# Kernel optimization log

Hardware: AMD Instinct MI355X
Metric: run time of the kernel (lower is better)

The kernel has to match this reference:

```python
import jax, jax.numpy as jnp
import numpy as np
from functools import partial

TAU = 2.0
EPS = 1e-5

@jax.custom_vjp
def spike(x):
    # Heaviside spike (x >= 0 -> 1). Surrogate sigmoid grad (alpha=4), matching spikingjelly default.
    return (x >= 0).astype(x.dtype)

def _spike_fwd(x):
    return (x >= 0).astype(x.dtype), x

def _spike_bwd(x, g):
    s = jax.nn.sigmoid(4.0 * x)
    return (4.0 * s * (1.0 - s) * g,)

spike.defvjp(_spike_fwd, _spike_bwd)

def lif(x, v_threshold=1.0):
    # Multi-step LIF over leading time axis. v_reset=0, hard reset, detach_reset.
    def step(v, xt):
        v = v + (xt - v) / TAU
        s = spike(v - v_threshold)
        v = v * (1.0 - jax.lax.stop_gradient(s))  # detached hard reset
        return v, s
    _, s = jax.lax.scan(step, jnp.zeros_like(x[0]), x)
    return s

def bn(x, gamma, beta):
    # BatchNorm1d in training mode over (T*B, C, N): stats over axes (T,B,N) per channel.
    m = x.mean(axis=(0, 1, 3), keepdims=True)
    v = x.var(axis=(0, 1, 3), keepdims=True)
    return (x - m) * jax.lax.rsqrt(v + EPS) * gamma[None, None, :, None] + beta[None, None, :, None]

def conv1x1(x, w, b=None):
    # 1x1 conv1d == channel-mixing GEMM. x: [T,B,C,N], w: [O,C]
    y = jnp.einsum('oc,tbcn->tbon', w, x)
    if b is not None:
        y = y + b[None, None, :, None]
    return y

def setup_inputs() -> dict:
    key = jax.random.key(0)
    ks = jax.random.split(key, 16)
    T, B, C, H, W = 4, 16, 512, 16, 16
    sc = 1.0 / np.sqrt(C)
    inp = {
        'x': jax.random.normal(ks[0], (T, B, C, H, W), dtype=jnp.float32),
        'q_w': jax.random.normal(ks[1], (C, C), dtype=jnp.float32) * sc,
        'q_gamma': jnp.ones((C,), jnp.float32), 'q_beta': jnp.zeros((C,), jnp.float32),
        'k_w': jax.random.normal(ks[2], (C, C), dtype=jnp.float32) * sc,
        'k_gamma': jnp.ones((C,), jnp.float32), 'k_beta': jnp.zeros((C,), jnp.float32),
        'v_w': jax.random.normal(ks[3], (C, C), dtype=jnp.float32) * sc,
        'v_gamma': jnp.ones((C,), jnp.float32), 'v_beta': jnp.zeros((C,), jnp.float32),
        'proj_w': jax.random.normal(ks[4], (C, C), dtype=jnp.float32) * sc,
        'proj_b': jnp.zeros((C,), jnp.float32),
        'proj_gamma': jnp.ones((C,), jnp.float32), 'proj_beta': jnp.zeros((C,), jnp.float32),
    }
    return inp

def reference(x, q_w, q_gamma, q_beta, k_w, k_gamma, k_beta, v_w, v_gamma, v_beta,
              proj_w, proj_b, proj_gamma, proj_beta):
    num_heads = 8
    scale = 0.125
    T, B, C, H, W = x.shape
    N = H * W
    d = C // num_heads
    xf = x.reshape(T, B, C, N)

    def branch(w, gamma, beta):
        s = lif(bn(conv1x1(xf, w), gamma, beta))          # [T,B,C,N] spikes
        # -> [T,B,heads,N,d]
        return s.transpose(0, 1, 3, 2).reshape(T, B, N, num_heads, d).transpose(0, 1, 3, 2, 4)

    q = branch(q_w, q_gamma, q_beta)
    k = branch(k_w, k_gamma, k_beta)
    v = branch(v_w, v_gamma, v_beta)

    kv = jnp.einsum('tbhnd,tbhne->tbhde', k, v)           # [T,B,h,d,d]
    attn = jnp.einsum('tbhnd,tbhde->tbhne', q, kv) * scale  # [T,B,h,N,d]
    attn = attn.transpose(0, 1, 2, 4, 3).reshape(T, B, C, N)
    attn = lif(attn, v_threshold=0.5)

    out = bn(conv1x1(attn, proj_w, proj_b), proj_gamma, proj_beta)
    out = lif(out.reshape(T, B, C, H, W))
    return out
```

## Files before the change

kernel.cpp:

```cpp
#include <hip/hip_runtime.h>
#include <hip/hip_bf16.h>
#include <stdint.h>

#define BCN  (16*512*256)
#define CN   (512*256)
#define NG   64
#define CAP  65536

typedef __attribute__((ext_vector_type(8))) short bf16x8;
typedef __attribute__((ext_vector_type(4))) float f32x4;
typedef __attribute__((ext_vector_type(4))) int   int4v;
typedef unsigned char u8;

__device__ inline ushort f2bf(float x){ union{ __hip_bfloat16 b; ushort u; } z; z.b = __float2bfloat16(x); return z.u; }
__device__ inline float  bf2f(ushort u){ union{ uint i; float f; } z; z.i = (uint)u<<16; return z.f; }

__device__ inline double blk_reduce(double v, double* sh){
  int tid = threadIdx.x; sh[tid] = v; __syncthreads();
  for (int off=128; off>0; off>>=1){ if (tid<off) sh[tid]+=sh[tid+off]; __syncthreads(); }
  double r = sh[0]; __syncthreads(); return r;
}

__global__ __launch_bounds__(256) void guard_fill(float* out, int n){
  int i = blockIdx.x*256+threadIdx.x; if (i<n) out[i] = -1.0f;
}

__global__ __launch_bounds__(256) void w_split(const float* __restrict__ W,
                                               ushort* __restrict__ Whi, ushort* __restrict__ Wlo){
  int i = blockIdx.x*256+threadIdx.x; if (i >= 512*512) return;
  float x = W[i]; ushort h = f2bf(x);
  Whi[i] = h; Wlo[i] = f2bf(x - bf2f(h));
}

__global__ __launch_bounds__(256) void wnorm_k(const float* __restrict__ W, double* __restrict__ wn){
  __shared__ double sh[256];
  int o = blockIdx.x;
  double s = 0.0;
  for (int c = threadIdx.x; c < 512; c += 256){ double w = (double)W[o*512+c]; s += w*w; }
  double t = blk_reduce(s, sh);
  if (threadIdx.x==0) wn[o] = sqrt(t);
}

__global__ __launch_bounds__(256) void xtrans32(const float* __restrict__ X, float* __restrict__ XT){
  __shared__ float lds[64][65];
  const int g = blockIdx.z, c0 = blockIdx.y<<6, n0 = blockIdx.x<<6;
  const int t = threadIdx.x, r = t>>2, q = t&3;
  #pragma unroll
  for (int u4=0; u4<4; ++u4){
    f32x4 v = *(const f32x4*)&X[((size_t)g*512 + c0 + r)*256 + n0 + q*16 + u4*4];
    lds[r][q*16+u4*4+0]=v.x; lds[r][q*16+u4*4+1]=v.y; lds[r][q*16+u4*4+2]=v.z; lds[r][q*16+u4*4+3]=v.w;
  }
  __syncthreads();
  #pragma unroll
  for (int u4=0; u4<4; ++u4){
    f32x4 o;
    o.x = lds[q*16+u4*4+0][r]; o.y = lds[q*16+u4*4+1][r];
    o.z = lds[q*16+u4*4+2][r]; o.w = lds[q*16+u4*4+3][r];
    *(f32x4*)&XT[((size_t)g*256 + n0 + r)*512 + c0 + q*16 + u4*4] = o;
  }
}

__global__ __launch_bounds__(256) void u8_trans(const u8* __restrict__ S, u8* __restrict__ ST){
  __shared__ u8 lds[64][65];
  const int g = blockIdx.z, c0 = blockIdx.y<<6, n0 = blockIdx.x<<6;
  const int t = threadIdx.x, r = t>>2, q = t&3;
  int4v v = *(const int4v*)&S[((size_t)g*512 + c0 + r)*256 + n0 + q*16];
  const u8* pb = (const u8*)&v;
  #pragma unroll
  for (int u=0; u<16; ++u) lds[r][q*16+u] = pb[u];
  __syncthreads();
  u8 ob[16];
  #pragma unroll
  for (int u=0; u<16; ++u) ob[u] = lds[q*16+u][r];
  *(int4v*)&ST[((size_t)g*256 + n0 + r)*512 + c0 + q*16] = *(int4v*)ob;
}

template<typename T>
__global__ __launch_bounds__(256) void colsum_k(const T* __restrict__ X, double* __restrict__ cs){
  __shared__ double sh[256];
  const int c = blockIdx.x;
  double s = 0.0;
  for (int g=0; g<NG; ++g) s += (double)X[((size_t)g*512+c)*256 + threadIdx.x];
  double t = blk_reduce(s, sh);
  if (threadIdx.x==0) cs[c] = t;
}

template<typename T>
__global__ __launch_bounds__(256) void norm_k2(const T* __restrict__ X, double* __restrict__ nrm){
  __shared__ double sh[4][64];
  const int g = blockIdx.x>>2, nq = blockIdx.x&3;
  const int nl = threadIdx.x&63, cg = threadIdx.x>>6;
  const int n = nq*64 + nl;
  double s = 0.0;
  #pragma unroll 4
  for (int c=cg; c<512; c+=4){
    double v = (double)X[((size_t)g*512+c)*256 + n]; s += v*v;
  }
  sh[cg][nl] = s; __syncthreads();
  if (cg==0) nrm[g*256+n] = sqrt(sh[0][nl]+sh[1][nl]+sh[2][nl]+sh[3][nl]);
}

__global__ __launch_bounds__(256, 4) void gramx2t(const float* __restrict__ X, double* __restrict__ Gpart){
  const int ti_tab[36] = {0,1,1,2,2,2,3,3,3,3,4,4,4,4,4,5,5,5,5,5,5,6,6,6,6,6,6,6,7,7,7,7,7,7,7,7};
  const int tj_tab[36] = {0,0,1,0,1,2,0,1,2,3,0,1,2,3,4,0,1,2,3,4,5,0,1,2,3,4,5,6,0,1,2,3,4,5,6,7};
  const int p = blockIdx.x, z = blockIdx.y;
  const int ci0 = ti_tab[p]<<6, cj0 = tj_tab[p]<<6;
  const bool offd = (ci0 != cj0);
  const int tid = threadIdx.x, tx = tid&15, ty = tid>>4;
  __shared__ float A[64][68];
  __shared__ float B[64][68];
  double acc[4][4] = {};

  for (int gg=0; gg<4; ++gg){
    const int g = z*4+gg;
    for (int nc=0; nc<4; ++nc){
      const int n0 = nc<<6;
      __syncthreads();
      { const int r = tid>>2, q = tid&3;
        #pragma unroll
        for (int u=0; u<4; ++u){
          f32x4 va = *(const f32x4*)&X[((size_t)g*512 + ci0 + r)*256 + n0 + q*16 + u*4];
          A[q*16+u*4+0][r]=va.x; A[q*16+u*4+1][r]=va.y; A[q*16+u*4+2][r]=va.z; A[q*16+u*4+3][r]=va.w;
          f32x4 vb = *(const f32x4*)&X[((size_t)g*512 + cj0 + r)*256 + n0 + q*16 + u*4];
          B[q*16+u*4+0][r]=vb.x; B[q*16+u*4+1][r]=vb.y; B[q*16+u*4+2][r]=vb.z; B[q*16+u*4+3][r]=vb.w;
        }
      }
      __syncthreads();
      #pragma unroll 8
      for (int n=0; n<64; ++n){
        const f32x4 af = *(const f32x4*)&A[n][ty*4];
        const f32x4 bf = *(const f32x4*)&B[n][tx*4];
        double a[4] = {(double)af.x,(double)af.y,(double)af.z,(double)af.w};
        double b[4] = {(double)bf.x,(double)bf.y,(double)bf.z,(double)bf.w};
        #pragma unroll
        for (int i=0;i<4;++i)
          #pragma unroll
          for (int j=0;j<4;++j) acc[i][j] = fma(a[i], b[j], acc[i][j]);
      }
    }
  }
  double* Gp = Gpart + (size_t)z*262144;
  #pragma unroll
  for (int i=0;i<4;++i)
    #pragma unroll
    for (int j=0;j<4;++j){
      Gp[(size_t)(ci0+ty*4+i)*512 + cj0+tx*4+j] = acc[i][j];
      if (offd) Gp[(size_t)(cj0+tx*4+j)*512 + ci0+ty*4+i] = acc[i][j];
    }
}

__global__ __launch_bounds__(256) void greduce64(const double* __restrict__ Gpart, double* __restrict__ G){
  const int i = blockIdx.x*256 + threadIdx.x;
  double s = 0.0;
  #pragma unroll
  for (int z=0; z<16; ++z) s += Gpart[(size_t)z*262144 + i];
  G[i] = s;
}

__global__ __launch_bounds__(256) void greduceS(const float* __restrict__ Gspart, float* __restrict__ Gs){
  const int i = blockIdx.x*256 + threadIdx.x;
  float s = 0.0f;
  #pragma unroll
  for (int z=0; z<16; ++z) s += Gspart[(size_t)z*262144 + i];
  Gs[i] = s;
}

template<typename GT>
__global__ __launch_bounds__(256) void mgemm(const float* __restrict__ W, const GT* __restrict__ G,
                                             double* __restrict__ M){
  const int o0 = blockIdx.y<<6, c0 = blockIdx.x<<6;
  const int k0base = blockIdx.z*128;
  __shared__ float  wT[32][68];
  __shared__ double gS[32][66];
  double acc[4][4];
  #pragma unroll
  for (int i=0;i<4;++i)
    #pragma unroll
    for (int j=0;j<4;++j) acc[i][j]=0.0;
  const int tid = threadIdx.x, tx = tid&15, ty = tid>>4;

  for (int kc=0; kc<4; ++kc){
    const int k0 = k0base + kc*32;
    __syncthreads();
    { int r = tid>>2, q = tid&3;
      f32x4 w0 = *(const f32x4*)&W[(size_t)(o0+r)*512 + k0 + q*8];
      f32x4 w1 = *(const f32x4*)&W[(size_t)(o0+r)*512 + k0 + q*8 + 4];
      wT[q*8+0][r]=w0.x; wT[q*8+1][r]=w0.y; wT[q*8+2][r]=w0.z; wT[q*8+3][r]=w0.w;
      wT[q*8+4][r]=w1.x; wT[q*8+5][r]=w1.y; wT[q*8+6][r]=w1.z; wT[q*8+7][r]=w1.w;
      int k = tid>>3, h = tid&7;
      #pragma unroll
      for (int u=0;u<8;++u) gS[k][h*8+u] = (double)G[(size_t)(k0+k)*512 + c0 + h*8 + u];
    }
    __syncthreads();
    #pragma unroll
    for (int k=0;k<32;++k){
      f32x4 aw = *(const f32x4*)&wT[k][ty*4];
      double a[4] = {(double)aw.x,(double)aw.y,(double)aw.z,(double)aw.w};
      double b[4];
      #pragma unroll
      for (int j=0;j<4;++j) b[j] = gS[k][tx*4+j];
      #pragma unroll
      for (int i=0;i<4;++i)
        #pragma unroll
        for (int j=0;j<4;++j) acc[i][j] = fma(a[i], b[j], acc[i][j]);
    }
  }
  #pragma unroll
  for (int i=0;i<4;++i)
    #pragma unroll
    for (int j=0;j<4;++j)
      atomicAdd(&M[(size_t)(o0+ty*4+i)*512 + c0+tx*4+j], acc[i][j]);
}

__global__ __launch_bounds__(256) void finalize_stats(const float* __restrict__ W, const double* __restrict__ M,
                                                      const double* __restrict__ cs,
                                                      const float* __restrict__ gamma, const float* __restrict__ beta,
                                                      double* __restrict__ stats){
  __shared__ double sh[256];
  const int o = blockIdx.x;
  double s1=0.0, s2=0.0;
  for (int c = threadIdx.x; c < 512; c += 256){
    double w = (double)W[(size_t)o*512+c];
    s1 += w*cs[c]; s2 += w*M[(size_t)o*512+c];
  }
  double t1 = blk_reduce(s1, sh);
  double t2 = blk_reduce(s2, sh);
  if (threadIdx.x==0){
    double mean = t1*(1.0/16384.0);
    double var  = t2*(1.0/16384.0) - mean*mean;
    double sc = (double)gamma[o] / sqrt(var + 1e-5);
    stats[o] = sc; stats[512+o] = (double)beta[o] - mean*sc;
  }
}

template<int MODE>
__global__ __launch_bounds__(256) void fgemm(const ushort* __restrict__ Ahi, const ushort* __restrict__ Alo,
                                             const void* __restrict__ Bsrc, float* __restrict__ Y){
  const int g = blockIdx.z, o0 = blockIdx.y<<7, n0 = blockIdx.x<<7;
  const int tid = threadIdx.x, lane = tid&63, wv = tid>>6;
  const int wo = (wv>>1)<<6, wn2 = (wv&1)<<6;
  const int l15 = lane&15, l4 = lane>>4, ss = l4 ^ (lane&3);
  __shared__ __align__(16) ushort L[4][128][32];
  f32x4 acc[4][4];
  #pragma unroll
  for (int i=0;i<4;++i)
    #pragma unroll
    for (int j=0;j<4;++j) acc[i][j] = f32x4{0.f,0.f,0.f,0.f};

  for (int c0=0; c0<512; c0+=32){
    __syncthreads();
    #pragma unroll
    for (int s2=0; s2<2; ++s2){
      int S = tid*2+s2, r = S>>2, q = S&3, qq = q ^ (r&3);
      *(int4v*)&L[0][r][qq*8] = *(const int4v*)&Ahi[(size_t)(o0+r)*512 + c0 + q*8];
      *(int4v*)&L[1][r][qq*8] = *(const int4v*)&Alo[(size_t)(o0+r)*512 + c0 + q*8];
      if (MODE==0){
        const float* B = (const float*)Bsrc;
        f32x4 x0 = *(const f32x4*)&B[((size_t)g*256 + n0 + r)*512 + c0 + q*8];
        f32x4 x1 = *(const f32x4*)&B[((size_t)g*256 + n0 + r)*512 + c0 + q*8 + 4];
        union { ushort us[8]; int4v v; } hiU, loU;
        float xv[8] = {x0.x,x0.y,x0.z,x0.w,x1.x,x1.y,x1.z,x1.w};
        #pragma unroll
        for (int u=0;u<8;++u){ ushort h = f2bf(xv[u]); hiU.us[u]=h; loU.us[u]=f2bf(xv[u]-bf2f(h)); }
        *(int4v*)&L[2][r][qq*8] = hiU.v;
        *(int4v*)&L[3][r][qq*8] = loU.v;
      } else {
        const u8* B = (const u8*)Bsrc;
        uint2 raw = *(const uint2*)&B[((size_t)g*256 + n0 + r)*512 + c0 + q*8];
        union { ushort us[8]; int4v v; } hiU;
        #pragma unroll
        for (int u=0;u<4;++u) hiU.us[u]   = ((raw.x>>(8*u))&255u) ? 0x3F80 : 0;
        #pragma unroll
        for (int u=0;u<4;++u) hiU.us[4+u] = ((raw.y>>(8*u))&255u) ? 0x3F80 : 0;
        *(int4v*)&L[2][r][qq*8] = hiU.v;
      }
    }
    __syncthreads();
    bf16x8 ah[4], al[4], bh[4], bl[4];
    #pragma unroll
    for (int f=0; f<4; ++f){
      int ra = wo + f*16 + l15;
      ah[f] = *(const bf16x8*)&L[0][ra][ss*8];
      al[f] = *(const bf16x8*)&L[1][ra][ss*8];
      int rb = wn2 + f*16 + l15;
      bh[f] = *(const bf16x8*)&L[2][rb][ss*8];
      if (MODE==0) bl[f] = *(const bf16x8*)&L[3][rb][ss*8];
    }
    #pragma unroll
    for (int of=0; of<4; ++of)
      #pragma unroll
      for (int nf=0; nf<4; ++nf){
        acc[of][nf] = __builtin_amdgcn_mfma_f32_16x16x32_bf16(ah[of], bh[nf], acc[of][nf], 0,0,0);
        acc[of][nf] = __builtin_amdgcn_mfma_f32_16x16x32_bf16(al[of], bh[nf], acc[of][nf], 0,0,0);
        if (MODE==0)
          acc[of][nf] = __builtin_amdgcn_mfma_f32_16x16x32_bf16(ah[of], bl[nf], acc[of][nf], 0,0,0);
      }
  }
  #pragma unroll
  for (int of=0; of<4; ++of)
    #pragma unroll
    for (int nf=0; nf<4; ++nf){
      #pragma unroll
      for (int r=0;r<4;++r){
        int o = o0 + wo + of*16 + l4*4 + r;
        int n = n0 + wn2 + nf*16 + l15;
        Y[((size_t)g*512 + o)*256 + n] = acc[of][nf][r];
      }
    }
}

__global__ __launch_bounds__(256) void sgram(const u8* __restrict__ S, float* __restrict__ Gspart){
  const int ci0 = blockIdx.x<<7, cj0 = blockIdx.y<<7, slice = blockIdx.z;
  const int tid = threadIdx.x, lane = tid&63, wv = tid>>6;
  const int wo = (wv>>1)<<6, wn2 = (wv&1)<<6;
  const int l15 = lane&15, l4 = lane>>4, ss = l4 ^ (lane&3);
  __shared__ __align__(16) ushort L[2][128][32];
  f32x4 acc[4][4];
  #pragma unroll
  for (int i=0;i<4;++i)
    #pragma unroll
    for (int j=0;j<4;++j) acc[i][j] = f32x4{0.f,0.f,0.f,0.f};

  for (int gg=0; gg<4; ++gg){
    const int g = slice*4+gg;
    for (int nc=0; nc<8; ++nc){
      const int n0 = nc*32;
      __syncthreads();
      #pragma unroll
      for (int s2=0; s2<2; ++s2){
        int Sl = tid*2+s2, r = Sl>>2, q = Sl&3, qq = q ^ (r&3);
        uint2 ra = *(const uint2*)&S[((size_t)g*512 + ci0 + r)*256 + n0 + q*8];
        uint2 rb = *(const uint2*)&S[((size_t)g*512 + cj0 + r)*256 + n0 + q*8];
        union { ushort us[8]; int4v v; } A, Bv;
        #pragma unroll
        for (int u=0;u<4;++u){ A.us[u]   = ((ra.x>>(8*u))&255u)?0x3F80:0; Bv.us[u]   = ((rb.x>>(8*u))&255u)?0x3F80:0; }
        #pragma unroll
        for (int u=0;u<4;++u){ A.us[4+u] = ((ra.y>>(8*u))&255u)?0x3F80:0; Bv.us[4+u] = ((rb.y>>(8*u))&255u)?0x3F80:0; }
        *(int4v*)&L[0][r][qq*8] = A.v;
        *(int4v*)&L[1][r][qq*8] = Bv.v;
      }
      __syncthreads();
      bf16x8 af[4], bfv[4];
      #pragma unroll
      for (int f=0; f<4; ++f){
        int ra = wo + f*16 + l15;  af[f]  = *(const bf16x8*)&L[0][ra][ss*8];
        int rb = wn2 + f*16 + l15; bfv[f] = *(const bf16x8*)&L[1][rb][ss*8];
      }
      #pragma unroll
      for (int of=0; of<4; ++of)
        #pragma unroll
        for (int nf=0; nf<4; ++nf)
          acc[of][nf] = __builtin_amdgcn_mfma_f32_16x16x32_bf16(af[of], bfv[nf], acc[of][nf], 0,0,0);
    }
  }
  float* Gp = Gspart + (size_t)slice*262144;
  #pragma unroll
  for (int of=0; of<4; ++of)
    #pragma unroll
    for (int nf=0; nf<4; ++nf)
      #pragma unroll
      for (int r=0;r<4;++r){
        int ci = ci0 + wo + of*16 + l4*4 + r;
        int cj = cj0 + wn2 + nf*16 + l15;
        Gp[(size_t)ci*512 + cj] = acc[of][nf][r];
      }
}

template<int OUTF>
__global__ __launch_bounds__(256) void bn_lif_flag(const float* __restrict__ Y, const double* __restrict__ stats,
                                                   const double* __restrict__ wn, const double* __restrict__ xn,
                                                   double K, void* __restrict__ sout,
                                                   uint* __restrict__ list, int* __restrict__ cnt){
  const int idx = blockIdx.x*256 + threadIdx.x;
  const int n = idx & 255, o = (idx>>8) & 511, b = idx>>17;
  const double scale = stats[o], shift = stats[512+o];
  const double kw = K * fabs(scale) * wn[o];
  double v = 0.0, minm = 1e300, bmax = 0.0;
  #pragma unroll
  for (int t=0;t<4;++t){
    const int g = t*16+b;
    const size_t ii = ((size_t)g*512+o)*256 + n;
    double y = (double)Y[ii];
    double Bnd = kw * xn[g*256+n]; bmax = fmax(bmax, Bnd);
    double z = y*scale + shift;
    v = v + (z - v)*0.5;
    double m = fabs(v - 1.0) - 2.0*bmax;
    minm = fmin(minm, m);
    bool sp = (v - 1.0) >= 0.0;
    if (OUTF) ((float*)sout)[ii] = sp ? 1.0f : 0.0f;
    else      ((u8*)sout)[ii]    = sp ? 1 : 0;
    if (sp) v = 0.0;
  }
  if (minm < 0.0){
    int pos = atomicAdd(cnt, 1);
    if (pos < CAP) list[pos] = ((uint)b<<17)|((uint)o<<8)|(uint)n;
  }
}

template<int OUTF>
__global__ __launch_bounds__(256) void recompute(const uint* __restrict__ list, const int* __restrict__ cnt,
                                                 const float* __restrict__ W, const void* __restrict__ Xn,
                                                 const double* __restrict__ stats, void* __restrict__ out){
  const int lane = threadIdx.x & 63;
  const int wv = blockIdx.x*4 + (threadIdx.x>>6);
  int ne = *cnt; if (ne > CAP) ne = CAP;
  for (int e = wv; e < ne; e += gridDim.x*4){
    const uint code = list[e];
    const int b = code>>17, o = (code>>8)&511, n = code&255;
    if (b > 15) continue;
    const double scale = stats[o], shift = stats[512+o];
    double v = 0.0;
    for (int t=0;t<4;++t){
      const int g = t*16+b;
      double y = 0.0;
      #pragma unroll
      for (int i=0;i<8;++i){
        int c = lane + 64*i;
        double w = (double)W[(size_t)o*512 + c];
        double xv;
        if (OUTF) xv = (double)((const u8*)Xn)[((size_t)g*256+n)*512 + c];
        else      xv = (double)((const float*)Xn)[((size_t)g*256+n)*512 + c];
        y = fma(w, xv, y);
      }
      #pragma unroll
      for (int off=32; off>0; off>>=1) y += __shfl_xor(y, off);
      double z = y*scale + shift;
      v = v + (z - v)*0.5;
      bool sp = (v - 1.0) >= 0.0;
      if (lane==0){
        const size_t ii = ((size_t)g*512+o)*256 + n;
        if (OUTF) ((float*)out)[ii] = sp ? 1.0f : 0.0f;
        else      ((u8*)out)[ii]    = sp ? 1 : 0;
      }
      if (sp) v = 0.0;
    }
  }
}

__global__ __launch_bounds__(256) void lif_kernel(const float* __restrict__ Y, double thresh,
                                                  u8* __restrict__ s_u8){
  const size_t idx = (size_t)blockIdx.x * 256 + threadIdx.x;
  double v = 0.0;
  #pragma unroll
  for (int t = 0; t < 4; ++t){
    double z = (double)Y[(size_t)t * BCN + idx];
    v = v + (z - v) * 0.5;
    bool sp = (v - thresh) >= 0.0;
    s_u8[(size_t)t * BCN + idx] = sp ? 1 : 0;
    if (sp) v = 0.0;
  }
}

__global__ __launch_bounds__(256) void attn_kv(const u8* __restrict__ sk, const u8* __restrict__ sv,
                                               float* __restrict__ kv){
  const int blk = blockIdx.x;
  const int tid = threadIdx.x;
  const size_t base = ((size_t)(blk >> 3) * 512 + (size_t)(blk & 7) * 64) * 256;
  __shared__ u8 kS[64][256];
  __shared__ u8 vS[64][256];
  const uint32_t* K32 = (const uint32_t*)(sk + base);
  const uint32_t* V32 = (const uint32_t*)(sv + base);
  uint32_t* kS32 = (uint32_t*)&kS[0][0];
  uint32_t* vS32 = (uint32_t*)&vS[0][0];
  #pragma unroll
  for (int i = 0; i < 16; ++i){ kS32[i*256+tid] = K32[i*256+tid]; vS32[i*256+tid] = V32[i*256+tid]; }
  __syncthreads();
  const int d0 = (tid >> 4) << 2, e0 = (tid & 15) << 2;
  int acc[4][4] = {};
  for (int n = 0; n < 256; ++n){
    int k_[4], v_[4];
    #pragma unroll
    for (int i = 0; i < 4; ++i) k_[i] = kS[d0+i][n];
    #pragma unroll
    for (int j = 0; j < 4; ++j) v_[j] = vS[e0+j][n];
    #pragma unroll
    for (int i = 0; i < 4; ++i)
      #pragma unroll
      for (int j = 0; j < 4; ++j) acc[i][j] += k_[i]*v_[j];
  }
  float* KV = kv + (size_t)blk * 4096;
  #pragma unroll
  for (int i = 0; i < 4; ++i)
    #pragma unroll
    for (int j = 0; j < 4; ++j) KV[(d0+i)*64 + e0+j] = (float)acc[i][j];
}

__global__ __launch_bounds__(256) void attn_qkv(const u8* __restrict__ sq, const float* __restrict__ kv,
                                                float* __restrict__ attn){
  const int blk = blockIdx.x;
  const int tid = threadIdx.x;
  const size_t base = ((size_t)(blk >> 3) * 512 + (size_t)(blk & 7) * 64) * 256;
  __shared__ u8 qS[64][256];
  __shared__ float kvS[64][64];
  const uint32_t* Q32 = (const uint32_t*)(sq + base);
  uint32_t* qS32 = (uint32_t*)&qS[0][0];
  const float* KV = kv + (size_t)blk * 4096;
  #pragma unroll
  for (int i = 0; i < 16; ++i){
    qS32[i*256+tid] = Q32[i*256+tid];
    (&kvS[0][0])[i*256+tid] = KV[i*256+tid];
  }
  __syncthreads();
  const int n = tid;
  float acc[64];
  #pragma unroll
  for (int e = 0; e < 64; ++e) acc[e] = 0.0f;
  for (int d = 0; d < 64; ++d){
    float qf = (float)qS[d][n];
    #pragma unroll
    for (int e = 0; e < 64; ++e) acc[e] = fmaf(qf, kvS[d][e], acc[e]);
  }
  float* A = attn + base;
  #pragma unroll
  for (int e = 0; e < 64; ++e) A[(size_t)e*256 + n] = acc[e]*0.125f;
}

extern "C" void kernel_launch(void* const* d_in, const int* in_sizes, int n_in,
                              void* d_out, int out_size, void* d_ws, size_t ws_size,
                              hipStream_t stream){
  const float* x       = (const float*)d_in[0];
  const float* Wb[4]   = {(const float*)d_in[1], (const float*)d_in[4], (const float*)d_in[7], (const float*)d_in[10]};
  const float* Gm[4]   = {(const float*)d_in[2], (const float*)d_in[5], (const float*)d_in[8], (const float*)d_in[12]};
  const float* Bt[4]   = {(const float*)d_in[3], (const float*)d_in[6], (const float*)d_in[9], (const float*)d_in[13]};

  char* p = (char*)d_ws;
  float* yA   = (float*)p;            p += 33554432;
  u8* s_q     = (u8*)p;               p += 8388608;
  u8* s_k     = (u8*)p;               p += 8388608;
  u8* s_v     = (u8*)p;               p += 8388608;
  u8* s_at    = (u8*)p;               p += 8388608;
  float* XT32 = (float*)p;
  u8* sT      = (u8*)p;               p += 33554432;
  ushort* Whl = (ushort*)p;           p += 4194304;
  float* kvb  = (float*)p;            p += 8388608;
  double* G   = (double*)p;           p += 2097152;
  float* Gs   = (float*)p;            p += 1048576;
  double* M   = (double*)p;           p += 2097152;
  double* colsumX = (double*)p;       p += 4096;
  double* colsumS = (double*)p;       p += 4096;
  double* xnorm   = (double*)p;       p += 131072;
  double* snorm   = (double*)p;       p += 131072;
  double* wn      = (double*)p;       p += 16384;
  double* stats   = (double*)p;       p += 32768;
  int*    cnt     = (int*)p;          p += 256;
  uint*   lists   = (uint*)p;         p += 4*CAP*4;
  const size_t NEED = (size_t)(p - (char*)d_ws);

  double* Gpart  = (double*)yA;
  float*  Gspart = (float*)yA;

  if (ws_size < NEED){
    guard_fill<<<(out_size+255)/256, 256, 0, stream>>>((float*)d_out, out_size);
    return;
  }

  const double K0 = 4.0e-5;
  const double K1 = 4.0e-5;

  hipMemsetAsync(cnt, 0, 256, stream);

  for (int i=0;i<4;++i){
    w_split<<<1024, 256, 0, stream>>>(Wb[i], Whl + (size_t)i*524288, Whl + (size_t)i*524288 + 262144);
    wnorm_k<<<512, 256, 0, stream>>>(Wb[i], wn + i*512);
  }
  xtrans32<<<dim3(4,8,64), 256, 0, stream>>>(x, XT32);
  colsum_k<float><<<512, 256, 0, stream>>>(x, colsumX);
  norm_k2<float><<<256, 256, 0, stream>>>(x, xnorm);
  gramx2t<<<dim3(36,16), 256, 0, stream>>>(x, Gpart);
  greduce64<<<1024, 256, 0, stream>>>(Gpart, G);

  u8* sOut[3] = {s_q, s_k, s_v};
  for (int i=0;i<3;++i){
    hipMemsetAsync(M, 0, 2097152, stream);
    mgemm<double><<<dim3(8,8,4), 256, 0, stream>>>(Wb[i], G, M);
    finalize_stats<<<512, 256, 0, stream>>>(Wb[i], M, colsumX, Gm[i], Bt[i], stats + i*1024);
    fgemm<0><<<dim3(2,4,64), 256, 0, stream>>>(Whl + (size_t)i*524288, Whl + (size_t)i*524288 + 262144,
                                               XT32, yA);
    bn_lif_flag<0><<<8192, 256, 0, stream>>>(yA, stats + i*1024, wn + i*512, xnorm, K0,
                                             sOut[i], lists + (size_t)i*CAP, cnt + i);
    recompute<0><<<512, 256, 0, stream>>>(lists + (size_t)i*CAP, cnt + i, Wb[i], XT32, stats + i*1024, sOut[i]);
  }

  attn_kv<<<512, 256, 0, stream>>>(s_k, s_v, kvb);
  attn_qkv<<<512, 256, 0, stream>>>(s_q, kvb, yA);
  lif_kernel<<<8192, 256, 0, stream>>>(yA, 0.5, s_at);

  u8_trans<<<dim3(4,8,64), 256, 0, stream>>>(s_at, sT);
  colsum_k<u8><<<512, 256, 0, stream>>>(s_at, colsumS);
  norm_k2<u8><<<256, 256, 0, stream>>>(s_at, snorm);
  sgram<<<dim3(4,4,16), 256, 0, stream>>>(s_at, Gspart);
  greduceS<<<1024, 256, 0, stream>>>(Gspart, Gs);

  hipMemsetAsync(M, 0, 2097152, stream);
  mgemm<float><<<dim3(8,8,4), 256, 0, stream>>>(Wb[3], Gs, M);
  finalize_stats<<<512, 256, 0, stream>>>(Wb[3], M, colsumS, Gm[3], Bt[3], stats + 3*1024);
  fgemm<1><<<dim3(2,4,64), 256, 0, stream>>>(Whl + (size_t)3*524288, Whl + (size_t)3*524288 + 262144,
                                             sT, yA);
  bn_lif_flag<1><<<8192, 256, 0, stream>>>(yA, stats + 3*1024, wn + 3*512, snorm, K1,
                                           d_out, lists + (size_t)3*CAP, cnt + 3);
  recompute<1><<<512, 256, 0, stream>>>(lists + (size_t)3*CAP, cnt + 3, Wb[3], sT, stats + 3*1024, d_out);
}
```

Before: 1.006 ms.

## Widen Gram kernels' grid, use fp64 atomics, batch weight prep launches

```diff
diff --git a/kernel.cpp b/kernel.cpp
--- a/kernel.cpp
+++ b/kernel.cpp
@@ -25,20 +25,27 @@
   int i = blockIdx.x*256+threadIdx.x; if (i<n) out[i] = -1.0f;
 }
 
-__global__ __launch_bounds__(256) void w_split(const float* __restrict__ W,
-                                               ushort* __restrict__ Whi, ushort* __restrict__ Wlo){
-  int i = blockIdx.x*256+threadIdx.x; if (i >= 512*512) return;
+__global__ __launch_bounds__(256) void w_split4(const float* __restrict__ W0, const float* __restrict__ W1,
+                                                const float* __restrict__ W2, const float* __restrict__ W3,
+                                                ushort* __restrict__ Whl){
+  int gid = blockIdx.x*256+threadIdx.x;
+  int m = gid >> 18, i = gid & 262143;
+  const float* W = (m==0)?W0:(m==1)?W1:(m==2)?W2:W3;
   float x = W[i]; ushort h = f2bf(x);
-  Whi[i] = h; Wlo[i] = f2bf(x - bf2f(h));
-}
-
-__global__ __launch_bounds__(256) void wnorm_k(const float* __restrict__ W, double* __restrict__ wn){
+  Whl[(size_t)m*524288 + i] = h;
+  Whl[(size_t)m*524288 + 262144 + i] = f2bf(x - bf2f(h));
+}
+
+__global__ __launch_bounds__(256) void wnorm4(const float* __restrict__ W0, const float* __restrict__ W1,
+                                              const float* __restrict__ W2, const float* __restrict__ W3,
+                                              double* __restrict__ wn){
   __shared__ double sh[256];
-  int o = blockIdx.x;
+  const int m = blockIdx.x >> 9, o = blockIdx.x & 511;
+  const float* W = (m==0)?W0:(m==1)?W1:(m==2)?W2:W3;
   double s = 0.0;
   for (int c = threadIdx.x; c < 512; c += 256){ double w = (double)W[o*512+c]; s += w*w; }
   double t = blk_reduce(s, sh);
-  if (threadIdx.x==0) wn[o] = sqrt(t);
+  if (threadIdx.x==0) wn[m*512 + o] = sqrt(t);
 }
 
 __global__ __launch_bounds__(256) void xtrans32(const float* __restrict__ X, float* __restrict__ XT){
@@ -100,10 +107,10 @@
   if (cg==0) nrm[g*256+n] = sqrt(sh[0][nl]+sh[1][nl]+sh[2][nl]+sh[3][nl]);
 }
 
-__global__ __launch_bounds__(256, 4) void gramx2t(const float* __restrict__ X, double* __restrict__ Gpart){
+__global__ __launch_bounds__(256, 4) void gramx3(const float* __restrict__ X, double* __restrict__ G){
   const int ti_tab[36] = {0,1,1,2,2,2,3,3,3,3,4,4,4,4,4,5,5,5,5,5,5,6,6,6,6,6,6,6,7,7,7,7,7,7,7,7};
   const int tj_tab[36] = {0,0,1,0,1,2,0,1,2,3,0,1,2,3,4,0,1,2,3,4,5,0,1,2,3,4,5,6,0,1,2,3,4,5,6,7};
-  const int p = blockIdx.x, z = blockIdx.y;
+  const int p = blockIdx.x, g = blockIdx.y;
   const int ci0 = ti_tab[p]<<6, cj0 = tj_tab[p]<<6;
   const bool offd = (ci0 != cj0);
   const int tid = threadIdx.x, tx = tid&15, ty = tid>>4;
@@ -111,57 +118,45 @@
   __shared__ float B[64][68];
   double acc[4][4] = {};
 
-  for (int gg=0; gg<4; ++gg){
-    const int g = z*4+gg;
-    for (int nc=0; nc<4; ++nc){
-      const int n0 = nc<<6;
-      __syncthreads();
-      { const int r = tid>>2, q = tid&3;
-        #pragma unroll
-        for (int u=0; u<4; ++u){
-          f32x4 va = *(const f32x4*)&X[((size_t)g*512 + ci0 + r)*256 + n0 + q*16 + u*4];
-          A[q*16+u*4+0][r]=va.x; A[q*16+u*4+1][r]=va.y; A[q*16+u*4+2][r]=va.z; A[q*16+u*4+3][r]=va.w;
-          f32x4 vb = *(const f32x4*)&X[((size_t)g*512 + cj0 + r)*256 + n0 + q*16 + u*4];
-          B[q*16+u*4+0][r]=vb.x; B[q*16+u*4+1][r]=vb.y; B[q*16+u*4+2][r]=vb.z; B[q*16+u*4+3][r]=vb.w;
-        }
-      }
-      __syncthreads();
-      #pragma unroll 8
-      for (int n=0; n<64; ++n){
-        const f32x4 af = *(const f32x4*)&A[n][ty*4];
-        const f32x4 bf = *(const f32x4*)&B[n][tx*4];
-        double a[4] = {(double)af.x,(double)af.y,(double)af.z,(double)af.w};
-        double b[4] = {(double)bf.x,(double)bf.y,(double)bf.z,(double)bf.w};
-        #pragma unroll
-        for (int i=0;i<4;++i)
-          #pragma unroll
-          for (int j=0;j<4;++j) acc[i][j] = fma(a[i], b[j], acc[i][j]);
-      }
-    }
-  }
-  double* Gp = Gpart + (size_t)z*262144;
+  for (int nc=0; nc<4; ++nc){
+    const int n0 = nc<<6;
+    __syncthreads();
+    { const int r = tid>>2, q = tid&3;
+      #pragma unroll
+      for (int u=0; u<4; ++u){
+        f32x4 va = *(const f32x4*)&X[((size_t)g*512 + ci0 + r)*256 + n0 + q*16 + u*4];
+        A[q*16+u*4+0][r]=va.x; A[q*16+u*4+1][r]=va.y; A[q*16+u*4+2][r]=va.z; A[q*16+u*4+3][r]=va.w;
+        f32x4 vb = *(const f32x4*)&X[((size_t)g*512 + cj0 + r)*256 + n0 + q*16 + u*4];
+        B[q*16+u*4+0][r]=vb.x; B[q*16+u*4+1][r]=vb.y; B[q*16+u*4+2][r]=vb.z; B[q*16+u*4+3][r]=vb.w;
+      }
+    }
+    __syncthreads();
+    #pragma unroll 8
+    for (int n=0; n<64; ++n){
+      const f32x4 af = *(const f32x4*)&A[n][ty*4];
+      const f32x4 bf = *(const f32x4*)&B[n][tx*4];
+      double a[4] = {(double)af.x,(double)af.y,(double)af.z,(double)af.w};
+      double b[4] = {(double)bf.x,(double)bf.y,(double)bf.z,(double)bf.w};
+      #pragma unroll
+      for (int i=0;i<4;++i)
+        #pragma unroll
+        for (int j=0;j<4;++j) acc[i][j] = fma(a[i], b[j], acc[i][j]);
+    }
+  }
   #pragma unroll
   for (int i=0;i<4;++i)
     #pragma unroll
     for (int j=0;j<4;++j){
-      Gp[(size_t)(ci0+ty*4+i)*512 + cj0+tx*4+j] = acc[i][j];
-      if (offd) Gp[(size_t)(cj0+tx*4+j)*512 + ci0+ty*4+i] = acc[i][j];
-    }
-}
-
-__global__ __launch_bounds__(256) void greduce64(const double* __restrict__ Gpart, double* __restrict__ G){
-  const int i = blockIdx.x*256 + threadIdx.x;
-  double s = 0.0;
-  #pragma unroll
-  for (int z=0; z<16; ++z) s += Gpart[(size_t)z*262144 + i];
-  G[i] = s;
+      atomicAdd(&G[(size_t)(ci0+ty*4+i)*512 + cj0+tx*4+j], acc[i][j]);
+      if (offd) atomicAdd(&G[(size_t)(cj0+tx*4+j)*512 + ci0+ty*4+i], acc[i][j]);
+    }
 }
 
 __global__ __launch_bounds__(256) void greduceS(const float* __restrict__ Gspart, float* __restrict__ Gs){
   const int i = blockIdx.x*256 + threadIdx.x;
   float s = 0.0f;
   #pragma unroll
-  for (int z=0; z<16; ++z) s += Gspart[(size_t)z*262144 + i];
+  for (int z=0; z<32; ++z) s += Gspart[(size_t)z*262144 + i];
   Gs[i] = s;
 }
 
@@ -321,8 +316,8 @@
     #pragma unroll
     for (int j=0;j<4;++j) acc[i][j] = f32x4{0.f,0.f,0.f,0.f};
 
-  for (int gg=0; gg<4; ++gg){
-    const int g = slice*4+gg;
+  for (int gg=0; gg<2; ++gg){
+    const int g = slice*2+gg;
     for (int nc=0; nc<8; ++nc){
       const int n0 = nc*32;
       __syncthreads();
@@ -546,8 +541,7 @@
   uint*   lists   = (uint*)p;         p += 4*CAP*4;
   const size_t NEED = (size_t)(p - (char*)d_ws);
 
-  double* Gpart  = (double*)yA;
-  float*  Gspart = (float*)yA;
+  float* Gspart = (float*)yA;
 
   if (ws_size < NEED){
     guard_fill<<<(out_size+255)/256, 256, 0, stream>>>((float*)d_out, out_size);
@@ -558,16 +552,14 @@
   const double K1 = 4.0e-5;
 
   hipMemsetAsync(cnt, 0, 256, stream);
-
-  for (int i=0;i<4;++i){
-    w_split<<<1024, 256, 0, stream>>>(Wb[i], Whl + (size_t)i*524288, Whl + (size_t)i*524288 + 262144);
-    wnorm_k<<<512, 256, 0, stream>>>(Wb[i], wn + i*512);
-  }
+  hipMemsetAsync(G,   0, 2097152, stream);
+
+  w_split4<<<4096, 256, 0, stream>>>(Wb[0], Wb[1], Wb[2], Wb[3], Whl);
+  wnorm4<<<2048, 256, 0, stream>>>(Wb[0], Wb[1], Wb[2], Wb[3], wn);
   xtrans32<<<dim3(4,8,64), 256, 0, stream>>>(x, XT32);
   colsum_k<float><<<512, 256, 0, stream>>>(x, colsumX);
   norm_k2<float><<<256, 256, 0, stream>>>(x, xnorm);
-  gramx2t<<<dim3(36,16), 256, 0, stream>>>(x, Gpart);
-  greduce64<<<1024, 256, 0, stream>>>(Gpart, G);
+  gramx3<<<dim3(36,64), 256, 0, stream>>>(x, G);
 
   u8* sOut[3] = {s_q, s_k, s_v};
   for (int i=0;i<3;++i){
@@ -588,7 +580,7 @@
   u8_trans<<<dim3(4,8,64), 256, 0, stream>>>(s_at, sT);
   colsum_k<u8><<<512, 256, 0, stream>>>(s_at, colsumS);
   norm_k2<u8><<<256, 256, 0, stream>>>(s_at, snorm);
-  sgram<<<dim3(4,4,16), 256, 0, stream>>>(s_at, Gspart);
+  sgram<<<dim3(4,4,32), 256, 0, stream>>>(s_at, Gspart);
   greduceS<<<1024, 256, 0, stream>>>(Gspart, Gs);
 
   hipMemsetAsync(M, 0, 2097152, stream);
```

Result: slower. 1.227 ms (+21.9%).
